# Optimization experiments

Hardware: AMD Instinct MI355X
Metric: run time of the kernel (lower is better)

## Reference

```python
import jax, jax.numpy as jnp
import numpy as np

B, T, H, C = 64, 512, 1024, 21  # batch, seq_len, hidden_size, num_labels


def setup_inputs() -> dict:
    key = jax.random.key(0)
    ks = jax.random.split(key, 7)
    hidden_states = jax.random.normal(ks[0], (B, T, H), dtype=jnp.float32)
    lengths = jax.random.randint(ks[1], (B,), 1, T + 1)  # at least 1 valid token
    attention_mask = jnp.arange(T)[None, :] < lengths[:, None]  # [B,T] bool, contiguous prefix
    labels = jax.random.randint(ks[2], (B, T), 0, C)
    # classifier params (nn.Linear(H, C))
    W = jax.random.normal(ks[3], (H, C), dtype=jnp.float32) * 0.02
    b = jnp.zeros((C,), dtype=jnp.float32)
    # CRF params (torchcrf init: uniform(-0.1, 0.1))
    transitions = jax.random.uniform(ks[4], (C, C), minval=-0.1, maxval=0.1, dtype=jnp.float32)
    start_transitions = jax.random.uniform(ks[5], (C,), minval=-0.1, maxval=0.1, dtype=jnp.float32)
    end_transitions = jax.random.uniform(ks[6], (C,), minval=-0.1, maxval=0.1, dtype=jnp.float32)
    return {
        "hidden_states": hidden_states,
        "W": W,
        "b": b,
        "transitions": transitions,
        "start_transitions": start_transitions,
        "end_transitions": end_transitions,
        "attention_mask": attention_mask,
        "labels": labels,
    }


def _crf_nll(emissions, tags, mask, transitions, start_transitions, end_transitions):
    """Mean negative log-likelihood of torchcrf CRF(batch_first=True, reduction='mean')."""
    maskf = mask.astype(emissions.dtype)
    # ---- numerator: score of the gold tag path ----
    em_tag = jnp.take_along_axis(emissions, tags[..., None], axis=2)[..., 0]  # [B,T]
    trans_score = transitions[tags[:, :-1], tags[:, 1:]]                      # [B,T-1]
    num = (start_transitions[tags[:, 0]] + em_tag[:, 0]
           + jnp.sum((trans_score + em_tag[:, 1:]) * maskf[:, 1:], axis=1))
    last_idx = jnp.sum(mask.astype(jnp.int32), axis=1) - 1                    # [B]
    last_tag = jnp.take_along_axis(tags, last_idx[:, None], axis=1)[:, 0]
    num = num + end_transitions[last_tag]
    # ---- denominator: forward algorithm (log partition) ----
    alpha0 = start_transitions[None, :] + emissions[:, 0]                     # [B,C]

    def step(alpha, xs):
        em_t, m_t = xs  # [B,C], [B]
        nxt = jax.nn.logsumexp(alpha[:, :, None] + transitions[None, :, :] + em_t[:, None, :], axis=1)
        return jnp.where(m_t[:, None], nxt, alpha), None

    xs = (jnp.swapaxes(emissions[:, 1:], 0, 1), jnp.swapaxes(mask[:, 1:], 0, 1))
    alphaT, _ = jax.lax.scan(step, alpha0, xs)
    logZ = jax.nn.logsumexp(alphaT + end_transitions[None, :], axis=1)        # [B]
    llh = num - logZ
    return -jnp.mean(llh)


def reference(hidden_states, W, b, transitions, start_transitions, end_transitions,
              attention_mask, labels):
    # dropout is identity at inference; emissions = Linear(hidden)
    emissions = jnp.einsum('bth,hc->btc', hidden_states, W) + b              # [B,T,C]
    # mask logic from the module: attention_mask & (labels != -100); mask[:,0] = True
    mask = attention_mask & (labels != -100)
    mask = mask.at[:, 0].set(True)
    loss = _crf_nll(emissions, labels, mask, transitions, start_transitions, end_transitions)
    return emissions, loss
```

## Files before the change

### kernel.cpp

```cpp
#include <hip/hip_runtime.h>

#define BB 64
#define TT 512
#define HH 1024
#define CC 21
#define NROWS (BB*TT)

__global__ __launch_bounds__(256) void emis_gemm(const float* __restrict__ hs,
                                                 const float* __restrict__ W,
                                                 const float* __restrict__ bias,
                                                 float* __restrict__ out) {
  __shared__ float lds[5376];
  const int tid  = threadIdx.x;
  const int lane = tid & 63;
  const int row0 = blockIdx.x * 64;
  const int sub  = __builtin_amdgcn_readfirstlane(tid >> 6);

  if (blockIdx.x == 0 && tid == 0) out[(size_t)NROWS * CC] = 0.f;

  float acc[CC];
#pragma unroll
  for (int c = 0; c < CC; ++c) acc[c] = 0.f;

  float4 buf[4];
#pragma unroll
  for (int i = 0; i < 4; ++i) {
    int l4 = tid + i * 256;
    int r = l4 >> 4, c4 = l4 & 15;
    buf[i] = *reinterpret_cast<const float4*>(hs + (size_t)(row0 + r) * HH + c4 * 4);
  }
#pragma unroll
  for (int i = 0; i < 4; ++i) {
    int l4 = tid + i * 256;
    int r = l4 >> 4, c4 = l4 & 15;
    lds[r * 65 + c4 * 4 + 0] = buf[i].x;
    lds[r * 65 + c4 * 4 + 1] = buf[i].y;
    lds[r * 65 + c4 * 4 + 2] = buf[i].z;
    lds[r * 65 + c4 * 4 + 3] = buf[i].w;
  }
  __syncthreads();

  for (int chunk = 0; chunk < 16; ++chunk) {
    const int k0 = chunk * 64;
    if (chunk < 15) {
#pragma unroll
      for (int i = 0; i < 4; ++i) {
        int l4 = tid + i * 256;
        int r = l4 >> 4, c4 = l4 & 15;
        buf[i] = *reinterpret_cast<const float4*>(hs + (size_t)(row0 + r) * HH + (k0 + 64) + c4 * 4);
      }
    }
    const float* Wp = W + (size_t)(k0 + sub * 16) * CC;
#pragma unroll
    for (int kk = 0; kk < 16; ++kk) {
      float x = lds[lane * 65 + sub * 16 + kk];
#pragma unroll
      for (int c = 0; c < CC; ++c) acc[c] = fmaf(x, Wp[kk * CC + c], acc[c]);
    }
    __syncthreads();
    if (chunk < 15) {
#pragma unroll
      for (int i = 0; i < 4; ++i) {
        int l4 = tid + i * 256;
        int r = l4 >> 4, c4 = l4 & 15;
        lds[r * 65 + c4 * 4 + 0] = buf[i].x;
        lds[r * 65 + c4 * 4 + 1] = buf[i].y;
        lds[r * 65 + c4 * 4 + 2] = buf[i].z;
        lds[r * 65 + c4 * 4 + 3] = buf[i].w;
      }
      __syncthreads();
    }
  }

  if (sub > 0) {
#pragma unroll
    for (int c = 0; c < CC; ++c) lds[(sub - 1) * 1344 + lane * CC + c] = acc[c];
  }
  __syncthreads();
  if (sub == 0) {
#pragma unroll
    for (int c = 0; c < CC; ++c) {
      float v = acc[c] + lds[lane * CC + c] + lds[1344 + lane * CC + c]
                        + lds[2688 + lane * CC + c] + bias[c];
      lds[4032 + lane * CC + c] = v;
    }
  }
  __syncthreads();
  for (int idx = tid; idx < 1344; idx += 256)
    out[(size_t)row0 * CC + idx] = lds[4032 + idx];
}

__global__ __launch_bounds__(128) void crf_kernel(const float* __restrict__ em,
                                                  const float* __restrict__ trans,
                                                  const float* __restrict__ startT,
                                                  const float* __restrict__ endT,
                                                  const int* __restrict__ att,
                                                  const int* __restrict__ labels,
                                                  float* __restrict__ loss) {
  const int b    = blockIdx.x;
  const int tid  = threadIdx.x;
  const int wave = tid >> 6;
  const int lane = tid & 63;
  __shared__ float sh_num;
  __shared__ int   sh_len;

  const float L2E = 1.4426950408889634f;
  const float LN2 = 0.6931471805599453f;

  if (wave == 1) {
    int cnt = 0;
    for (int t = lane; t < TT; t += 64) {
      bool m = (t == 0) || ((att[b * TT + t] != 0) && (labels[b * TT + t] != -100));
      cnt += m ? 1 : 0;
    }
#pragma unroll
    for (int off = 32; off >= 1; off >>= 1) cnt += __shfl_down(cnt, off);
    cnt = __shfl(cnt, 0);

    float s = 0.f;
    for (int t = lane + 1; t < TT; t += 64) {
      bool m = (att[b * TT + t] != 0) && (labels[b * TT + t] != -100);
      if (m) {
        int tp = labels[b * TT + t - 1], tc = labels[b * TT + t];
        s += trans[tp * CC + tc] + em[((size_t)b * TT + t) * CC + tc];
      }
    }
#pragma unroll
    for (int off = 32; off >= 1; off >>= 1) s += __shfl_down(s, off);
    if (lane == 0) {
      int tag0 = labels[b * TT];
      int lastTag = labels[b * TT + cnt - 1];
      s += startT[tag0] + em[((size_t)b * TT) * CC + tag0] + endT[lastTag];
      sh_num = s;
      sh_len = cnt;
    }
  }

  const int j = lane < CC ? lane : CC - 1;
  float E[CC];
  float beta = 0.f, endE = 0.f;
  if (wave == 0) {
#pragma unroll
    for (int i = 0; i < CC; ++i)
      E[i] = __builtin_amdgcn_exp2f(trans[i * CC + j] * L2E);
    beta = __builtin_amdgcn_exp2f((startT[j] + em[((size_t)b * TT) * CC + j]) * L2E);
    endE = __builtin_amdgcn_exp2f(endT[j] * L2E);
  }
  __syncthreads();

  if (wave == 0) {
    const int len = sh_len;
    int ksum = 0;

    float sb[CC];
#pragma unroll
    for (int i = 0; i < CC; ++i)
      sb[i] = __int_as_float(__builtin_amdgcn_readlane(__float_as_int(beta), i));

    const float* emB = em + (size_t)b * TT * CC;
    auto clampi = [&](int t) { return t < len ? t : (len - 1); };
    float r0 = emB[(size_t)clampi(1) * CC + j];
    float r1 = emB[(size_t)clampi(2) * CC + j];
    float r2 = emB[(size_t)clampi(3) * CC + j];

    for (int t = 1; t < len; ++t) {
      float rn = emB[(size_t)clampi(t + 3) * CC + j];
      float pm = __builtin_amdgcn_exp2f(r0 * L2E);
      float c0 = 0.f, c1 = 0.f, c2 = 0.f;
#pragma unroll
      for (int i = 0; i < CC; i += 3) c0 = fmaf(sb[i], E[i], c0);
#pragma unroll
      for (int i = 1; i < CC; i += 3) c1 = fmaf(sb[i], E[i], c1);
#pragma unroll
      for (int i = 2; i < CC; i += 3) c2 = fmaf(sb[i], E[i], c2);
      float nxt = ((c0 + c1) + c2) * pm;
      int bits0 = __builtin_amdgcn_readlane(__float_as_int(nxt), 0);
      int e = ((bits0 >> 23) & 255) - 127;
      ksum += e;
      float scale = __int_as_float((127 - e) << 23);
      beta = nxt * scale;
#pragma unroll
      for (int i = 0; i < CC; ++i)
        sb[i] = __int_as_float(__builtin_amdgcn_readlane(__float_as_int(beta), i));
      r0 = r1; r1 = r2; r2 = rn;
    }

    float v = (lane < CC) ? beta * endE : 0.f;
#pragma unroll
    for (int off = 32; off >= 1; off >>= 1) v += __shfl_xor(v, off);
    if (lane == 0) {
      float logZ = (float)ksum * LN2 + LN2 * __builtin_amdgcn_logf(v);
      atomicAdd(loss, -(sh_num - logZ) * (1.0f / 64.0f));
    }
  }
}

extern "C" void kernel_launch(void* const* d_in, const int* in_sizes, int n_in,
                              void* d_out, int out_size, void* d_ws, size_t ws_size,
                              hipStream_t stream) {
  const float* hs     = (const float*)d_in[0];
  const float* W      = (const float*)d_in[1];
  const float* bias   = (const float*)d_in[2];
  const float* trans  = (const float*)d_in[3];
  const float* startT = (const float*)d_in[4];
  const float* endT   = (const float*)d_in[5];
  const int*   att    = (const int*)d_in[6];
  const int*   labels = (const int*)d_in[7];
  float* out = (float*)d_out;

  emis_gemm<<<dim3(512), dim3(256), 0, stream>>>(hs, W, bias, out);
  crf_kernel<<<dim3(64), dim3(128), 0, stream>>>(out, trans, startT, endT, att,
                                                 labels, out + (size_t)NROWS * CC);
}
```

Measured before the change: 333.4 us.

## Double-buffer GEMM LDS with 8-wave K split; shorten CRF recurrence critical path

The emission GEMM now runs 512 threads per block, with 8 waves each owning 8 k-columns per chunk. It double-buffers the hidden-state tile in LDS so the next chunk is written during compute with a single barrier per chunk, and reduces 8 partial sums at the end. The CRF forward loop takes its rescaling exponent from the previous step's beta, which is already broadcast, instead of reading back the new value. This removes a readlane from the serial dependency chain. Emission prefetch is deepened to 8 steps with an unrolled loop, at the cost of more LDS and registers and an 8-way final reduction.

```diff
diff --git a/kernel.cpp b/kernel.cpp
--- a/kernel.cpp
+++ b/kernel.cpp
@@ -6,15 +6,15 @@
 #define CC 21
 #define NROWS (BB*TT)
 
-__global__ __launch_bounds__(256) void emis_gemm(const float* __restrict__ hs,
+__global__ __launch_bounds__(512) void emis_gemm(const float* __restrict__ hs,
                                                  const float* __restrict__ W,
                                                  const float* __restrict__ bias,
                                                  float* __restrict__ out) {
-  __shared__ float lds[5376];
+  __shared__ float lds[17728];
   const int tid  = threadIdx.x;
   const int lane = tid & 63;
+  const int w    = __builtin_amdgcn_readfirstlane(tid >> 6);
   const int row0 = blockIdx.x * 64;
-  const int sub  = __builtin_amdgcn_readfirstlane(tid >> 6);
 
   if (blockIdx.x == 0 && tid == 0) out[(size_t)NROWS * CC] = 0.f;
 
@@ -22,72 +22,62 @@
 #pragma unroll
   for (int c = 0; c < CC; ++c) acc[c] = 0.f;
 
-  float4 buf[4];
-#pragma unroll
-  for (int i = 0; i < 4; ++i) {
-    int l4 = tid + i * 256;
-    int r = l4 >> 4, c4 = l4 & 15;
-    buf[i] = *reinterpret_cast<const float4*>(hs + (size_t)(row0 + r) * HH + c4 * 4);
-  }
-#pragma unroll
-  for (int i = 0; i < 4; ++i) {
-    int l4 = tid + i * 256;
-    int r = l4 >> 4, c4 = l4 & 15;
-    lds[r * 65 + c4 * 4 + 0] = buf[i].x;
-    lds[r * 65 + c4 * 4 + 1] = buf[i].y;
-    lds[r * 65 + c4 * 4 + 2] = buf[i].z;
-    lds[r * 65 + c4 * 4 + 3] = buf[i].w;
+  const int r_  = (tid) >> 4,        c4_  = tid & 15;
+  const int r2_ = (tid + 512) >> 4;
+
+  float4 buf0, buf1;
+  buf0 = *reinterpret_cast<const float4*>(hs + (size_t)(row0 + r_ ) * HH + c4_ * 4);
+  buf1 = *reinterpret_cast<const float4*>(hs + (size_t)(row0 + r2_) * HH + c4_ * 4);
+  {
+    float* t0 = &lds[r_  * 65 + c4_ * 4];
+    float* t1 = &lds[r2_ * 65 + c4_ * 4];
+    t0[0] = buf0.x; t0[1] = buf0.y; t0[2] = buf0.z; t0[3] = buf0.w;
+    t1[0] = buf1.x; t1[1] = buf1.y; t1[2] = buf1.z; t1[3] = buf1.w;
   }
   __syncthreads();
 
   for (int chunk = 0; chunk < 16; ++chunk) {
-    const int k0 = chunk * 64;
+    const int cur = (chunk & 1) * 4160;
+    const int nxt = ((chunk + 1) & 1) * 4160;
     if (chunk < 15) {
-#pragma unroll
-      for (int i = 0; i < 4; ++i) {
-        int l4 = tid + i * 256;
-        int r = l4 >> 4, c4 = l4 & 15;
-        buf[i] = *reinterpret_cast<const float4*>(hs + (size_t)(row0 + r) * HH + (k0 + 64) + c4 * 4);
-      }
-    }
-    const float* Wp = W + (size_t)(k0 + sub * 16) * CC;
-#pragma unroll
-    for (int kk = 0; kk < 16; ++kk) {
-      float x = lds[lane * 65 + sub * 16 + kk];
+      const int k0n = (chunk + 1) * 64;
+      buf0 = *reinterpret_cast<const float4*>(hs + (size_t)(row0 + r_ ) * HH + k0n + c4_ * 4);
+      buf1 = *reinterpret_cast<const float4*>(hs + (size_t)(row0 + r2_) * HH + k0n + c4_ * 4);
+    }
+    const float* Wp = W + (size_t)(chunk * 64 + w * 8) * CC;
+#pragma unroll
+    for (int kk = 0; kk < 8; ++kk) {
+      float x = lds[cur + lane * 65 + w * 8 + kk];
 #pragma unroll
       for (int c = 0; c < CC; ++c) acc[c] = fmaf(x, Wp[kk * CC + c], acc[c]);
     }
+    if (chunk < 15) {
+      float* t0 = &lds[nxt + r_  * 65 + c4_ * 4];
+      float* t1 = &lds[nxt + r2_ * 65 + c4_ * 4];
+      t0[0] = buf0.x; t0[1] = buf0.y; t0[2] = buf0.z; t0[3] = buf0.w;
+      t1[0] = buf1.x; t1[1] = buf1.y; t1[2] = buf1.z; t1[3] = buf1.w;
+    }
     __syncthreads();
-    if (chunk < 15) {
-#pragma unroll
-      for (int i = 0; i < 4; ++i) {
-        int l4 = tid + i * 256;
-        int r = l4 >> 4, c4 = l4 & 15;
-        lds[r * 65 + c4 * 4 + 0] = buf[i].x;
-        lds[r * 65 + c4 * 4 + 1] = buf[i].y;
-        lds[r * 65 + c4 * 4 + 2] = buf[i].z;
-        lds[r * 65 + c4 * 4 + 3] = buf[i].w;
-      }
-      __syncthreads();
-    }
-  }
-
-  if (sub > 0) {
-#pragma unroll
-    for (int c = 0; c < CC; ++c) lds[(sub - 1) * 1344 + lane * CC + c] = acc[c];
-  }
-  __syncthreads();
-  if (sub == 0) {
+  }
+
+  if (w > 0) {
+#pragma unroll
+    for (int c = 0; c < CC; ++c)
+      lds[8320 + (w - 1) * 1344 + lane * CC + c] = acc[c];
+  }
+  __syncthreads();
+  if (w == 0) {
 #pragma unroll
     for (int c = 0; c < CC; ++c) {
-      float v = acc[c] + lds[lane * CC + c] + lds[1344 + lane * CC + c]
-                        + lds[2688 + lane * CC + c] + bias[c];
-      lds[4032 + lane * CC + c] = v;
-    }
-  }
-  __syncthreads();
-  for (int idx = tid; idx < 1344; idx += 256)
-    out[(size_t)row0 * CC + idx] = lds[4032 + idx];
+      float v = acc[c] + bias[c];
+#pragma unroll
+      for (int q = 0; q < 7; ++q) v += lds[8320 + q * 1344 + lane * CC + c];
+      lds[lane * CC + c] = v;
+    }
+  }
+  __syncthreads();
+  for (int idx = tid; idx < 1344; idx += 512)
+    out[(size_t)row0 * CC + idx] = lds[idx];
 }
 
 __global__ __launch_bounds__(128) void crf_kernel(const float* __restrict__ em,
@@ -158,14 +148,12 @@
       sb[i] = __int_as_float(__builtin_amdgcn_readlane(__float_as_int(beta), i));
 
     const float* emB = em + (size_t)b * TT * CC;
-    auto clampi = [&](int t) { return t < len ? t : (len - 1); };
-    float r0 = emB[(size_t)clampi(1) * CC + j];
-    float r1 = emB[(size_t)clampi(2) * CC + j];
-    float r2 = emB[(size_t)clampi(3) * CC + j];
-
-    for (int t = 1; t < len; ++t) {
-      float rn = emB[(size_t)clampi(t + 3) * CC + j];
-      float pm = __builtin_amdgcn_exp2f(r0 * L2E);
+
+    auto step = [&](float em_v) {
+      float pm = __builtin_amdgcn_exp2f(em_v * L2E);
+      int ef = (__float_as_int(sb[0]) >> 23) & 255;
+      ksum += ef - 127;
+      float pms = pm * __int_as_float((254 - ef) << 23);
       float c0 = 0.f, c1 = 0.f, c2 = 0.f;
 #pragma unroll
       for (int i = 0; i < CC; i += 3) c0 = fmaf(sb[i], E[i], c0);
@@ -173,16 +161,33 @@
       for (int i = 1; i < CC; i += 3) c1 = fmaf(sb[i], E[i], c1);
 #pragma unroll
       for (int i = 2; i < CC; i += 3) c2 = fmaf(sb[i], E[i], c2);
-      float nxt = ((c0 + c1) + c2) * pm;
-      int bits0 = __builtin_amdgcn_readlane(__float_as_int(nxt), 0);
-      int e = ((bits0 >> 23) & 255) - 127;
-      ksum += e;
-      float scale = __int_as_float((127 - e) << 23);
-      beta = nxt * scale;
+      beta = ((c0 + c1) + c2) * pms;
 #pragma unroll
       for (int i = 0; i < CC; ++i)
         sb[i] = __int_as_float(__builtin_amdgcn_readlane(__float_as_int(beta), i));
-      r0 = r1; r1 = r2; r2 = rn;
+    };
+
+    float r[8];
+#pragma unroll
+    for (int u = 0; u < 8; ++u) {
+      int tt = 1 + u; if (tt > len - 1) tt = len - 1;
+      r[u] = emB[(size_t)tt * CC + j];
+    }
+
+    int t = 1;
+    for (; t + 8 <= len; t += 8) {
+#pragma unroll
+      for (int u = 0; u < 8; ++u) {
+        int tp = t + u + 8; if (tp > len - 1) tp = len - 1;
+        float rn = emB[(size_t)tp * CC + j];
+        step(r[u]);
+        r[u] = rn;
+      }
+    }
+    for (; t < len; ++t) {
+      step(r[0]);
+#pragma unroll
+      for (int u = 0; u < 7; ++u) r[u] = r[u + 1];
     }
 
     float v = (lane < CC) ? beta * endE : 0.f;
@@ -208,7 +213,7 @@
   const int*   labels = (const int*)d_in[7];
   float* out = (float*)d_out;
 
-  emis_gemm<<<dim3(512), dim3(256), 0, stream>>>(hs, W, bias, out);
+  emis_gemm<<<dim3(512), dim3(512), 0, stream>>>(hs, W, bias, out);
   crf_kernel<<<dim3(64), dim3(128), 0, stream>>>(out, trans, startT, endT, att,
                                                  labels, out + (size_t)NROWS * CC);
 }
```

New measurement: 296.7 us. 11.0% less time.
